# Optimization experiments

Hardware: AMD Instinct MI355X
Metric: run time of the kernel (lower is better)

The kernel has to match this reference:

```python
import jax, jax.numpy as jnp
import numpy as np

DEGREE = 3


def bspline_basis(t, knots, degree):
    """Vectorized Cox-de Boor recursion. t: [S], knots: [K]. Returns B: [S, K-degree-1].
    Faithful to the torch loop: at degree d only columns [0, n_knots-d) are updated;
    higher columns keep their stale lower-degree values, and term2 reads the
    not-yet-updated column i+1 (i.e. previous-degree values), matching ascending-i
    in-place updates.
    """
    n_knots = knots.shape[0] - degree - 1
    # degree-0 basis: indicator of half-open knot spans
    B = ((knots[None, :n_knots] <= t[:, None]) &
         (t[:, None] < knots[None, 1:n_knots + 1])).astype(t.dtype)
    for d in range(1, degree + 1):
        n = n_knots - d
        denom1 = knots[d:d + n] - knots[:n]          # knots[i+d]   - knots[i]
        denom2 = knots[d + 1:d + 1 + n] - knots[1:1 + n]  # knots[i+d+1] - knots[i+1]
        safe1 = jnp.where(denom1 == 0, 1.0, denom1)
        safe2 = jnp.where(denom2 == 0, 1.0, denom2)
        w1 = jnp.where(denom1 == 0, 0.0, (t[:, None] - knots[None, :n]) / safe1)
        w2 = jnp.where(denom2 == 0, 0.0, (knots[None, d + 1:d + 1 + n] - t[:, None]) / safe2)
        new_cols = w1 * B[:, :n] + w2 * B[:, 1:n + 1]
        B = B.at[:, :n].set(new_cols)
    return B


def setup_inputs() -> dict:
    key = jax.random.key(0)
    k1, k2 = jax.random.split(key)
    N_KNOTS, DIM, T_MAX = 2048, 512, 32768.0
    t = jnp.sort(jax.random.uniform(k1, (N_KNOTS,), dtype=jnp.float32)) * T_MAX
    t = t.at[-1].set(T_MAX)  # make sample range exactly [0, T_MAX)
    c = jax.random.normal(k2, (DIM, N_KNOTS), dtype=jnp.float32)
    return {"t": t, "c": c, "delta": 1}


def reference(t, c, delta):
    padded_t = jnp.concatenate([jnp.zeros(DEGREE + 1, dtype=t.dtype), t])
    # number of samples is data-dependent (t[-1]); concretize outside jit
    t_max = float(t[-1])
    sample_points = jnp.arange(0.0, t_max, float(delta), dtype=t.dtype)  # [S]
    B = bspline_basis(sample_points, padded_t, DEGREE)  # [S, n_knots]
    spline_values = B @ c.T  # [S, dim]
    return sample_points, spline_values
```

## Files before the change

### kernel.cpp

```cpp
#include <hip/hip_runtime.h>


#define DEG 3

typedef float vfloat4 __attribute__((ext_vector_type(4)));

__device__ __forceinline__ float kn(const float* __restrict__ t, int i) {
    return (i < DEG + 1) ? 0.0f : t[i - (DEG + 1)];
}

#define TILE 32
__global__ __launch_bounds__(256) void prep_kernel(
    const float* __restrict__ c, float* __restrict__ cT,
    const float* __restrict__ t, const int* __restrict__ delta_p,
    float* __restrict__ out_pts, int* __restrict__ jbuf,
    vfloat4* __restrict__ bbuf, int S, int NK, int DIM, int TB)
{
    if ((int)blockIdx.x < TB) {
        __shared__ float tile[TILE][TILE + 1];
        int bx = blockIdx.x % (NK / TILE);
        int by = blockIdx.x / (NK / TILE);
        int tx = threadIdx.x % TILE;
        int ty = threadIdx.x / TILE;
        int x = bx * TILE + tx;
        int y = by * TILE + ty;
        #pragma unroll
        for (int i = 0; i < TILE; i += 8)
            tile[ty + i][tx] = c[(size_t)(y + i) * NK + x];
        __syncthreads();
        int x2 = by * TILE + tx;
        int y2 = bx * TILE + ty;
        #pragma unroll
        for (int i = 0; i < TILE; i += 8)
            cT[(size_t)(y2 + i) * DIM + x2] = tile[tx][ty + i];
        return;
    }

    int s = (blockIdx.x - TB) * blockDim.x + threadIdx.x;
    if (s >= S) return;
    const float delta = (float)(*delta_p);
    const float sv = (float)s * delta;
    out_pts[s] = sv;

    int lo = DEG, hi = NK + DEG - 1;
    while (lo < hi) {
        int mid = (lo + hi + 1) >> 1;
        if (kn(t, mid) <= sv) lo = mid; else hi = mid - 1;
    }
    const int j = lo;

    if (j >= NK) {
        jbuf[s] = NK - 1;
        bbuf[s] = (vfloat4){0.f, 0.f, 0.f, 0.f};
        return;
    }

    float N[DEG + 1][DEG + 1];
    N[0][0] = 1.0f;
    #pragma unroll
    for (int d = 1; d <= DEG; ++d) {
        #pragma unroll
        for (int k = 0; k <= d; ++k) {
            int i = j - d + k;
            float vpi  = (k >= 1) ? N[d - 1][k - 1] : 0.0f;
            float vpi1 = (k <= d - 1) ? N[d - 1][k] : 0.0f;
            float ki   = kn(t, i);
            float kid  = kn(t, i + d);
            float ki1  = kn(t, i + 1);
            float kid1 = kn(t, i + d + 1);
            float den1 = kid - ki;
            float den2 = kid1 - ki1;
            float w1 = (den1 != 0.0f) ? (sv - ki) / den1 : 0.0f;
            float w2 = (den2 != 0.0f) ? (kid1 - sv) / den2 : 0.0f;
            N[d][k] = w1 * vpi + w2 * vpi1;
        }
    }

    float b[DEG + 1];
    #pragma unroll
    for (int m = 0; m <= DEG; ++m) {
        int col = j - DEG + m;
        int deg = NK - 1 - col; if (deg > DEG) deg = DEG;
        int idx = m - DEG + deg;
        b[m] = (idx >= 0) ? N[deg][idx] : 0.0f;
    }
    jbuf[s] = j;
    bbuf[s] = (vfloat4){b[0], b[1], b[2], b[3]};
}

__device__ __forceinline__ vfloat4 dot4(const vfloat4 b, const vfloat4 a0,
                                        const vfloat4 a1, const vfloat4 a2,
                                        const vfloat4 a3) {
    return b.x * a0 + b.y * a1 + b.z * a2 + b.w * a3;
}

__global__ __launch_bounds__(256) void bspline_eval(
    const int* __restrict__ jbuf, const vfloat4* __restrict__ bbuf,
    const float* __restrict__ cT, vfloat4* __restrict__ out_spline,
    int DIM)
{
    const int nvec = DIM >> 2;
    int gtid = blockIdx.x * blockDim.x + threadIdx.x;
    int wid  = gtid >> 6;
    int lane = gtid & 63;
    int s0   = __builtin_amdgcn_readfirstlane(wid << 3);

    int j[8];
    vfloat4 b[8];
    #pragma unroll
    for (int m = 0; m < 8; ++m) { j[m] = jbuf[s0 + m]; b[m] = bbuf[s0 + m]; }

    vfloat4* orow = out_spline + (size_t)s0 * nvec + lane;

    if (j[0] == j[7]) {
        const vfloat4* r = (const vfloat4*)(cT + (size_t)(j[0] - 3) * DIM) + lane;
        vfloat4 a0 = r[0],        a0b = r[64];
        vfloat4 a1 = r[nvec],     a1b = r[nvec + 64];
        vfloat4 a2 = r[2 * nvec], a2b = r[2 * nvec + 64];
        vfloat4 a3 = r[3 * nvec], a3b = r[3 * nvec + 64];
        #pragma unroll
        for (int m = 0; m < 8; ++m) {
            __builtin_nontemporal_store(dot4(b[m], a0,  a1,  a2,  a3 ), orow + m * nvec);
            __builtin_nontemporal_store(dot4(b[m], a0b, a1b, a2b, a3b), orow + m * nvec + 64);
        }
    } else {
        #pragma unroll
        for (int h = 0; h < 2; ++h) {
            const int m0 = h * 4;
            if (j[m0] == j[m0 + 3]) {
                const vfloat4* r = (const vfloat4*)(cT + (size_t)(j[m0] - 3) * DIM) + lane;
                vfloat4 a0 = r[0],        a0b = r[64];
                vfloat4 a1 = r[nvec],     a1b = r[nvec + 64];
                vfloat4 a2 = r[2 * nvec], a2b = r[2 * nvec + 64];
                vfloat4 a3 = r[3 * nvec], a3b = r[3 * nvec + 64];
                #pragma unroll
                for (int m = m0; m < m0 + 4; ++m) {
                    __builtin_nontemporal_store(dot4(b[m], a0,  a1,  a2,  a3 ), orow + m * nvec);
                    __builtin_nontemporal_store(dot4(b[m], a0b, a1b, a2b, a3b), orow + m * nvec + 64);
                }
            } else {
                #pragma unroll
                for (int m = m0; m < m0 + 4; ++m) {
                    const vfloat4* r = (const vfloat4*)(cT + (size_t)(j[m] - 3) * DIM) + lane;
                    vfloat4 a0 = r[0],        a0b = r[64];
                    vfloat4 a1 = r[nvec],     a1b = r[nvec + 64];
                    vfloat4 a2 = r[2 * nvec], a2b = r[2 * nvec + 64];
                    vfloat4 a3 = r[3 * nvec], a3b = r[3 * nvec + 64];
                    __builtin_nontemporal_store(dot4(b[m], a0,  a1,  a2,  a3 ), orow + m * nvec);
                    __builtin_nontemporal_store(dot4(b[m], a0b, a1b, a2b, a3b), orow + m * nvec + 64);
                }
            }
        }
    }
}

extern "C" void kernel_launch(void* const* d_in, const int* in_sizes, int n_in,
                              void* d_out, int out_size, void* d_ws, size_t ws_size,
                              hipStream_t stream) {
    const float* t = (const float*)d_in[0];
    const float* c = (const float*)d_in[1];
    const int* delta = (const int*)d_in[2];
    const int NK = in_sizes[0];
    const int DIM = in_sizes[1] / NK;
    const int S = out_size / (1 + DIM);

    float* cT = (float*)d_ws;
    int* jbuf = (int*)((char*)d_ws + (size_t)NK * DIM * 4);
    vfloat4* bbuf = (vfloat4*)((char*)jbuf + (size_t)S * 4);

    const int TB = (NK / TILE) * (DIM / TILE);
    const int WB = (S + 255) / 256;
    prep_kernel<<<TB + WB, 256, 0, stream>>>(
        c, cT, t, delta, (float*)d_out, jbuf, bbuf, S, NK, DIM, TB);

    int total_threads = (S >> 3) * 64;
    bspline_eval<<<total_threads / 256, 256, 0, stream>>>(
        jbuf, bbuf, cT, (vfloat4*)((float*)d_out + S), DIM);
}
```

Before: 94.16 us.

## Fuse basis computation into eval kernel and broadcast weights via wave shuffles

Moves the knot binary search and Cox-de Boor weight computation out of the prep kernel and into the evaluation kernel. Within each wave, the 8 lanes whose index mod 8 matches compute the span and weights for their sample, and the results are broadcast with __shfl. This removes the jbuf/bbuf round trip through global memory and leaves the prep kernel as a pure transpose. In exchange, each wave repeats the binary search redundantly across its 64 lanes (8 copies per sample), which adds latency before the stores.

```diff
diff --git a/kernel.cpp b/kernel.cpp
--- a/kernel.cpp
+++ b/kernel.cpp
@@ -10,82 +10,25 @@
 }
 
 #define TILE 32
-__global__ __launch_bounds__(256) void prep_kernel(
-    const float* __restrict__ c, float* __restrict__ cT,
-    const float* __restrict__ t, const int* __restrict__ delta_p,
-    float* __restrict__ out_pts, int* __restrict__ jbuf,
-    vfloat4* __restrict__ bbuf, int S, int NK, int DIM, int TB)
+__global__ __launch_bounds__(256) void transpose_kernel(
+    const float* __restrict__ c, float* __restrict__ cT, int NK, int DIM)
 {
-    if ((int)blockIdx.x < TB) {
-        __shared__ float tile[TILE][TILE + 1];
-        int bx = blockIdx.x % (NK / TILE);
-        int by = blockIdx.x / (NK / TILE);
-        int tx = threadIdx.x % TILE;
-        int ty = threadIdx.x / TILE;
-        int x = bx * TILE + tx;
-        int y = by * TILE + ty;
-        #pragma unroll
-        for (int i = 0; i < TILE; i += 8)
-            tile[ty + i][tx] = c[(size_t)(y + i) * NK + x];
-        __syncthreads();
-        int x2 = by * TILE + tx;
-        int y2 = bx * TILE + ty;
-        #pragma unroll
-        for (int i = 0; i < TILE; i += 8)
-            cT[(size_t)(y2 + i) * DIM + x2] = tile[tx][ty + i];
-        return;
-    }
-
-    int s = (blockIdx.x - TB) * blockDim.x + threadIdx.x;
-    if (s >= S) return;
-    const float delta = (float)(*delta_p);
-    const float sv = (float)s * delta;
-    out_pts[s] = sv;
-
-    int lo = DEG, hi = NK + DEG - 1;
-    while (lo < hi) {
-        int mid = (lo + hi + 1) >> 1;
-        if (kn(t, mid) <= sv) lo = mid; else hi = mid - 1;
-    }
-    const int j = lo;
-
-    if (j >= NK) {
-        jbuf[s] = NK - 1;
-        bbuf[s] = (vfloat4){0.f, 0.f, 0.f, 0.f};
-        return;
-    }
-
-    float N[DEG + 1][DEG + 1];
-    N[0][0] = 1.0f;
+    __shared__ float tile[TILE][TILE + 1];
+    int bx = blockIdx.x % (NK / TILE);
+    int by = blockIdx.x / (NK / TILE);
+    int tx = threadIdx.x % TILE;
+    int ty = threadIdx.x / TILE;
+    int x = bx * TILE + tx;
+    int y = by * TILE + ty;
     #pragma unroll
-    for (int d = 1; d <= DEG; ++d) {
-        #pragma unroll
-        for (int k = 0; k <= d; ++k) {
-            int i = j - d + k;
-            float vpi  = (k >= 1) ? N[d - 1][k - 1] : 0.0f;
-            float vpi1 = (k <= d - 1) ? N[d - 1][k] : 0.0f;
-            float ki   = kn(t, i);
-            float kid  = kn(t, i + d);
-            float ki1  = kn(t, i + 1);
-            float kid1 = kn(t, i + d + 1);
-            float den1 = kid - ki;
-            float den2 = kid1 - ki1;
-            float w1 = (den1 != 0.0f) ? (sv - ki) / den1 : 0.0f;
-            float w2 = (den2 != 0.0f) ? (kid1 - sv) / den2 : 0.0f;
-            N[d][k] = w1 * vpi + w2 * vpi1;
-        }
-    }
-
-    float b[DEG + 1];
+    for (int i = 0; i < TILE; i += 8)
+        tile[ty + i][tx] = c[(size_t)(y + i) * NK + x];
+    __syncthreads();
+    int x2 = by * TILE + tx;
+    int y2 = bx * TILE + ty;
     #pragma unroll
-    for (int m = 0; m <= DEG; ++m) {
-        int col = j - DEG + m;
-        int deg = NK - 1 - col; if (deg > DEG) deg = DEG;
-        int idx = m - DEG + deg;
-        b[m] = (idx >= 0) ? N[deg][idx] : 0.0f;
-    }
-    jbuf[s] = j;
-    bbuf[s] = (vfloat4){b[0], b[1], b[2], b[3]};
+    for (int i = 0; i < TILE; i += 8)
+        cT[(size_t)(y2 + i) * DIM + x2] = tile[tx][ty + i];
 }
 
 __device__ __forceinline__ vfloat4 dot4(const vfloat4 b, const vfloat4 a0,
@@ -95,9 +38,9 @@
 }
 
 __global__ __launch_bounds__(256) void bspline_eval(
-    const int* __restrict__ jbuf, const vfloat4* __restrict__ bbuf,
-    const float* __restrict__ cT, vfloat4* __restrict__ out_spline,
-    int DIM)
+    const float* __restrict__ t, const int* __restrict__ delta_p,
+    const float* __restrict__ cT, float* __restrict__ out_pts,
+    vfloat4* __restrict__ out_spline, int NK, int DIM)
 {
     const int nvec = DIM >> 2;
     int gtid = blockIdx.x * blockDim.x + threadIdx.x;
@@ -105,10 +48,61 @@
     int lane = gtid & 63;
     int s0   = __builtin_amdgcn_readfirstlane(wid << 3);
 
+    const int m_my = lane & 7;
+    const int s_my = s0 + m_my;
+    const float delta = (float)(*delta_p);
+    const float sv = (float)s_my * delta;
+    if (lane < 8) out_pts[s_my] = sv;
+
+    int lo = DEG, hi = NK + DEG - 1;
+    while (lo < hi) {
+        int mid = (lo + hi + 1) >> 1;
+        if (kn(t, mid) <= sv) lo = mid; else hi = mid - 1;
+    }
+    int jj = lo;
+    float bw[DEG + 1];
+
+    if (jj >= NK) {
+        jj = NK - 1;
+        bw[0] = bw[1] = bw[2] = bw[3] = 0.0f;
+    } else {
+        float N[DEG + 1][DEG + 1];
+        N[0][0] = 1.0f;
+        #pragma unroll
+        for (int d = 1; d <= DEG; ++d) {
+            #pragma unroll
+            for (int k = 0; k <= d; ++k) {
+                int i = jj - d + k;
+                float vpi  = (k >= 1) ? N[d - 1][k - 1] : 0.0f;
+                float vpi1 = (k <= d - 1) ? N[d - 1][k] : 0.0f;
+                float ki   = kn(t, i);
+                float kid  = kn(t, i + d);
+                float ki1  = kn(t, i + 1);
+                float kid1 = kn(t, i + d + 1);
+                float den1 = kid - ki;
+                float den2 = kid1 - ki1;
+                float w1 = (den1 != 0.0f) ? (sv - ki) / den1 : 0.0f;
+                float w2 = (den2 != 0.0f) ? (kid1 - sv) / den2 : 0.0f;
+                N[d][k] = w1 * vpi + w2 * vpi1;
+            }
+        }
+        #pragma unroll
+        for (int m = 0; m <= DEG; ++m) {
+            int col = jj - DEG + m;
+            int deg = NK - 1 - col; if (deg > DEG) deg = DEG;
+            int idx = m - DEG + deg;
+            bw[m] = (idx >= 0) ? N[deg][idx] : 0.0f;
+        }
+    }
+
     int j[8];
     vfloat4 b[8];
     #pragma unroll
-    for (int m = 0; m < 8; ++m) { j[m] = jbuf[s0 + m]; b[m] = bbuf[s0 + m]; }
+    for (int m = 0; m < 8; ++m) {
+        j[m] = __shfl(jj, m);
+        b[m] = (vfloat4){__shfl(bw[0], m), __shfl(bw[1], m),
+                         __shfl(bw[2], m), __shfl(bw[3], m)};
+    }
 
     vfloat4* orow = out_spline + (size_t)s0 * nvec + lane;
 
@@ -165,15 +159,12 @@
     const int S = out_size / (1 + DIM);
 
     float* cT = (float*)d_ws;
-    int* jbuf = (int*)((char*)d_ws + (size_t)NK * DIM * 4);
-    vfloat4* bbuf = (vfloat4*)((char*)jbuf + (size_t)S * 4);
 
     const int TB = (NK / TILE) * (DIM / TILE);
-    const int WB = (S + 255) / 256;
-    prep_kernel<<<TB + WB, 256, 0, stream>>>(
-        c, cT, t, delta, (float*)d_out, jbuf, bbuf, S, NK, DIM, TB);
+    transpose_kernel<<<TB, 256, 0, stream>>>(c, cT, NK, DIM);
 
     int total_threads = (S >> 3) * 64;
     bspline_eval<<<total_threads / 256, 256, 0, stream>>>(
-        jbuf, bbuf, cT, (vfloat4*)((float*)d_out + S), DIM);
+        t, delta, cT, (float*)d_out,
+        (vfloat4*)((float*)d_out + S), NK, DIM);
 }
```

New measurement: 97.10 us. 3.1% more time.

## Read coefficients directly in original layout, drop transpose pass

Applied to the files above, without the earlier changes.

Removes the transpose of c into a [NK, DIM] workspace and has the eval kernel read c in its original [DIM, NK] layout. Each lane gathers four consecutive knot coefficients per output column. Each wave now covers half the columns, so twice as many waves run over 8 samples. This removes the transpose traffic and its fusion into the prep kernel, but the reads become strided: each lane touches a different row of c, roughly 8 KB apart, so the loads are uncoalesced and rely on cache for reuse.

```diff
diff --git a/kernel.cpp b/kernel.cpp
--- a/kernel.cpp
+++ b/kernel.cpp
@@ -9,34 +9,12 @@
     return (i < DEG + 1) ? 0.0f : t[i - (DEG + 1)];
 }
 
-#define TILE 32
-__global__ __launch_bounds__(256) void prep_kernel(
-    const float* __restrict__ c, float* __restrict__ cT,
+__global__ __launch_bounds__(256) void weights_kernel(
     const float* __restrict__ t, const int* __restrict__ delta_p,
     float* __restrict__ out_pts, int* __restrict__ jbuf,
-    vfloat4* __restrict__ bbuf, int S, int NK, int DIM, int TB)
+    vfloat4* __restrict__ bbuf, int S, int NK)
 {
-    if ((int)blockIdx.x < TB) {
-        __shared__ float tile[TILE][TILE + 1];
-        int bx = blockIdx.x % (NK / TILE);
-        int by = blockIdx.x / (NK / TILE);
-        int tx = threadIdx.x % TILE;
-        int ty = threadIdx.x / TILE;
-        int x = bx * TILE + tx;
-        int y = by * TILE + ty;
-        #pragma unroll
-        for (int i = 0; i < TILE; i += 8)
-            tile[ty + i][tx] = c[(size_t)(y + i) * NK + x];
-        __syncthreads();
-        int x2 = by * TILE + tx;
-        int y2 = bx * TILE + ty;
-        #pragma unroll
-        for (int i = 0; i < TILE; i += 8)
-            cT[(size_t)(y2 + i) * DIM + x2] = tile[tx][ty + i];
-        return;
-    }
-
-    int s = (blockIdx.x - TB) * blockDim.x + threadIdx.x;
+    int s = blockIdx.x * blockDim.x + threadIdx.x;
     if (s >= S) return;
     const float delta = (float)(*delta_p);
     const float sv = (float)s * delta;
@@ -88,70 +66,70 @@
     bbuf[s] = (vfloat4){b[0], b[1], b[2], b[3]};
 }
 
-__device__ __forceinline__ vfloat4 dot4(const vfloat4 b, const vfloat4 a0,
-                                        const vfloat4 a1, const vfloat4 a2,
-                                        const vfloat4 a3) {
-    return b.x * a0 + b.y * a1 + b.z * a2 + b.w * a3;
-}
-
 __global__ __launch_bounds__(256) void bspline_eval(
     const int* __restrict__ jbuf, const vfloat4* __restrict__ bbuf,
-    const float* __restrict__ cT, vfloat4* __restrict__ out_spline,
-    int DIM)
+    const float* __restrict__ c, vfloat4* __restrict__ out_spline,
+    int NK, int DIM)
 {
     const int nvec = DIM >> 2;
     int gtid = blockIdx.x * blockDim.x + threadIdx.x;
     int wid  = gtid >> 6;
     int lane = gtid & 63;
-    int s0   = __builtin_amdgcn_readfirstlane(wid << 3);
+    int grp  = wid >> 1;
+    int half = wid & 1;
+    int s0   = __builtin_amdgcn_readfirstlane(grp << 3);
+    int col  = (half << 6) | lane;
 
     int j[8];
     vfloat4 b[8];
     #pragma unroll
     for (int m = 0; m < 8; ++m) { j[m] = jbuf[s0 + m]; b[m] = bbuf[s0 + m]; }
 
-    vfloat4* orow = out_spline + (size_t)s0 * nvec + lane;
+    const float* __restrict__ crow = c + (size_t)(4 * col) * NK;
+    vfloat4* orow = out_spline + (size_t)s0 * nvec + col;
+
+    vfloat4 o[8];
 
     if (j[0] == j[7]) {
-        const vfloat4* r = (const vfloat4*)(cT + (size_t)(j[0] - 3) * DIM) + lane;
-        vfloat4 a0 = r[0],        a0b = r[64];
-        vfloat4 a1 = r[nvec],     a1b = r[nvec + 64];
-        vfloat4 a2 = r[2 * nvec], a2b = r[2 * nvec + 64];
-        vfloat4 a3 = r[3 * nvec], a3b = r[3 * nvec + 64];
         #pragma unroll
-        for (int m = 0; m < 8; ++m) {
-            __builtin_nontemporal_store(dot4(b[m], a0,  a1,  a2,  a3 ), orow + m * nvec);
-            __builtin_nontemporal_store(dot4(b[m], a0b, a1b, a2b, a3b), orow + m * nvec + 64);
+        for (int k = 0; k < 4; ++k) {
+            const float* p = crow + (size_t)k * NK + (j[0] - 3);
+            float x0 = p[0], x1 = p[1], x2 = p[2], x3 = p[3];
+            #pragma unroll
+            for (int m = 0; m < 8; ++m)
+                o[m][k] = b[m].x * x0 + b[m].y * x1 + b[m].z * x2 + b[m].w * x3;
         }
     } else {
         #pragma unroll
         for (int h = 0; h < 2; ++h) {
             const int m0 = h * 4;
             if (j[m0] == j[m0 + 3]) {
-                const vfloat4* r = (const vfloat4*)(cT + (size_t)(j[m0] - 3) * DIM) + lane;
-                vfloat4 a0 = r[0],        a0b = r[64];
-                vfloat4 a1 = r[nvec],     a1b = r[nvec + 64];
-                vfloat4 a2 = r[2 * nvec], a2b = r[2 * nvec + 64];
-                vfloat4 a3 = r[3 * nvec], a3b = r[3 * nvec + 64];
                 #pragma unroll
-                for (int m = m0; m < m0 + 4; ++m) {
-                    __builtin_nontemporal_store(dot4(b[m], a0,  a1,  a2,  a3 ), orow + m * nvec);
-                    __builtin_nontemporal_store(dot4(b[m], a0b, a1b, a2b, a3b), orow + m * nvec + 64);
+                for (int k = 0; k < 4; ++k) {
+                    const float* p = crow + (size_t)k * NK + (j[m0] - 3);
+                    float x0 = p[0], x1 = p[1], x2 = p[2], x3 = p[3];
+                    #pragma unroll
+                    for (int m = m0; m < m0 + 4; ++m)
+                        o[m][k] = b[m].x * x0 + b[m].y * x1 + b[m].z * x2 + b[m].w * x3;
                 }
             } else {
                 #pragma unroll
-                for (int m = m0; m < m0 + 4; ++m) {
-                    const vfloat4* r = (const vfloat4*)(cT + (size_t)(j[m] - 3) * DIM) + lane;
-                    vfloat4 a0 = r[0],        a0b = r[64];
-                    vfloat4 a1 = r[nvec],     a1b = r[nvec + 64];
-                    vfloat4 a2 = r[2 * nvec], a2b = r[2 * nvec + 64];
-                    vfloat4 a3 = r[3 * nvec], a3b = r[3 * nvec + 64];
-                    __builtin_nontemporal_store(dot4(b[m], a0,  a1,  a2,  a3 ), orow + m * nvec);
-                    __builtin_nontemporal_store(dot4(b[m], a0b, a1b, a2b, a3b), orow + m * nvec + 64);
+                for (int k = 0; k < 4; ++k) {
+                    const float* p = crow + (size_t)k * NK;
+                    #pragma unroll
+                    for (int m = m0; m < m0 + 4; ++m) {
+                        const float* q = p + (j[m] - 3);
+                        o[m][k] = b[m].x * q[0] + b[m].y * q[1]
+                                + b[m].z * q[2] + b[m].w * q[3];
+                    }
                 }
             }
         }
     }
+
+    #pragma unroll
+    for (int m = 0; m < 8; ++m)
+        __builtin_nontemporal_store(o[m], orow + m * nvec);
 }
 
 extern "C" void kernel_launch(void* const* d_in, const int* in_sizes, int n_in,
@@ -164,16 +142,13 @@
     const int DIM = in_sizes[1] / NK;
     const int S = out_size / (1 + DIM);
 
-    float* cT = (float*)d_ws;
-    int* jbuf = (int*)((char*)d_ws + (size_t)NK * DIM * 4);
-    vfloat4* bbuf = (vfloat4*)((char*)jbuf + (size_t)S * 4);
+    int* jbuf = (int*)d_ws;
+    vfloat4* bbuf = (vfloat4*)((char*)d_ws + (size_t)S * 4);
 
-    const int TB = (NK / TILE) * (DIM / TILE);
-    const int WB = (S + 255) / 256;
-    prep_kernel<<<TB + WB, 256, 0, stream>>>(
-        c, cT, t, delta, (float*)d_out, jbuf, bbuf, S, NK, DIM, TB);
+    weights_kernel<<<(S + 255) / 256, 256, 0, stream>>>(
+        t, delta, (float*)d_out, jbuf, bbuf, S, NK);
 
-    int total_threads = (S >> 3) * 64;
+    int total_threads = (S >> 3) * 2 * 64;
     bspline_eval<<<total_threads / 256, 256, 0, stream>>>(
-        jbuf, bbuf, cT, (vfloat4*)((float*)d_out + S), DIM);
+        jbuf, bbuf, c, (vfloat4*)((float*)d_out + S), NK, DIM);
 }
```

New measurement: 107.1 us. 1.14x slower.
